# Performance work log

Measured on AMD Instinct MI355X. Metric: run time of the kernel, lower is better.

Reference implementation:

```python
import jax, jax.numpy as jnp
import numpy as np

B, N, C, Cn, M = 4, 4096, 32, 64, 64


def fps(event, npoint):
    """Farthest point sampling, faithful to farthest_point_sample_batch.
    Returns selected points in ORIGINAL index order (masked_select semantics).
    event: [B, n, c] -> [B, npoint, c]
    """
    b, n, c = event.shape
    bidx = jnp.arange(b)
    barycenter = jnp.mean(event, axis=1, keepdims=True)            # [B,1,c]
    d0 = jnp.sum((event - barycenter) ** 2, axis=-1)               # [B,n]
    farthest = jnp.argmax(d0, axis=1)                              # [B]
    distance = jnp.full((b, n), 1e10, dtype=event.dtype)
    sel = jnp.zeros((b, n), dtype=bool)

    def body(carry, _):
        distance, farthest, sel = carry
        sel = sel.at[bidx, farthest].set(True)
        centroid = jnp.take_along_axis(event, farthest[:, None, None], axis=1)  # [B,1,c]
        d = jnp.sum((event - centroid) ** 2, axis=-1)              # [B,n]
        distance = jnp.minimum(distance, d)
        farthest = jnp.argmax(distance, axis=1)
        return (distance, farthest, sel), None

    (distance, farthest, sel), _ = jax.lax.scan(
        body, (distance, farthest, sel), None, length=npoint)
    # masked_select keeps original index order: stable sort puts selected first
    order = jnp.argsort(~sel, axis=1, stable=True)[:, :npoint]     # [B,npoint]
    return jnp.take_along_axis(event, order[:, :, None], axis=1)   # [B,npoint,c]


def setup_inputs() -> dict:
    key = jax.random.key(0)
    ks = jax.random.split(key, 7)
    s = 0.1
    return {
        "events_feature": jax.random.normal(ks[0], (B, N, C), jnp.float32),
        "W_qs": jax.random.normal(ks[1], (Cn, C), jnp.float32) * s,
        "W_ks": jax.random.normal(ks[2], (Cn, C), jnp.float32) * s,
        "W_vs": jax.random.normal(ks[3], (Cn, C), jnp.float32) * s,
        "W_pe": jax.random.normal(ks[4], (Cn, C), jnp.float32) * s,
        "W_sa1": jax.random.normal(ks[5], (1, Cn), jnp.float32) * s,
        "W_sa2": jax.random.normal(ks[6], (C, Cn), jnp.float32) * s,
    }


def reference(events_feature, W_qs, W_ks, W_vs, W_pe, W_sa1, W_sa2):
    q = events_feature @ W_qs.T                                   # [B,N,Cn]
    k = events_feature @ W_ks.T                                   # [B,N,Cn]
    v = events_feature @ W_vs.T                                   # [B,N,Cn]

    # position encoding: pairwise diff to M FPS-sampled events, then C->Cn
    ev_m = fps(events_feature, M)                                 # [B,M,C]
    pe = events_feature[:, :, None, :] - ev_m[:, None, :, :]      # [B,N,M,C]
    pe = pe @ W_pe.T                                              # [B,N,M,Cn]

    k_m = fps(k, M)                                               # [B,M,Cn]
    v_m = fps(v, M)                                               # [B,M,Cn]

    # vector attention scores: (q - k_m + pe) -> scalar per (n,m)
    sa = q[:, :, None, :] - k_m[:, None, :, :] + pe               # [B,N,M,Cn]
    logits = jnp.squeeze(sa @ W_sa1.T, -1)                        # [B,N,M]
    scores = jax.nn.softmax(logits, axis=-1)                      # [B,N,M]

    # Original: matmul(scores[B,1,N,M], (v_multi+pe).permute->[B,Cn,M,N]) then
    # sum over last axis. Summing first over n' is the same math and avoids the
    # [B,Cn,N,N] intermediate: sum_{n'} v_multi = N * v_m; sum_{n'} pe.
    S = N * v_m + jnp.sum(pe, axis=1)                             # [B,M,Cn]
    attn = jnp.einsum('bnm,bmc->bnc', scores, S)                  # [B,N,Cn]
    return attn @ W_sa2.T                                         # [B,N,C]
```

## Files before the change

### kernel.cpp

```cpp
#include <hip/hip_runtime.h>

constexpr int N_ = 4096, C_ = 32, CN_ = 64, M_ = 64;
constexpr int TPB = 1024;
constexpr int RPT = 3, LPT = 1;
constexpr int NREG = RPT * TPB;
constexpr int NLDS = N_ - NREG;
constexpr int NWAVES = TPB / 64;
constexpr int NTPB = 256;
constexpr int NCHUNK = N_ / NTPB;

typedef float v2f  __attribute__((ext_vector_type(2)));
typedef float v16f __attribute__((ext_vector_type(16)));

#define PKFMA(acc, zz, cc) \
  asm("v_pk_fma_f32 %0, %1, %2, %0" : "+v"(acc) : "v"(zz), "s"(cc))

__device__ __forceinline__ unsigned fmap(float v) {
  unsigned u = __float_as_uint(v);
  u ^= (unsigned)((int)u >> 31) | 0x80000000u;
  return u;
}

__device__ __forceinline__ float rfl(float v) {
  return __uint_as_float(__builtin_amdgcn_readfirstlane(__float_as_uint(v)));
}

template <int CTRL, int RM>
__device__ __forceinline__ unsigned long long kmax_dpp(unsigned long long k) {
  int lo = (int)(unsigned)k, hi = (int)(unsigned)(k >> 32);
  int plo = __builtin_amdgcn_update_dpp(lo, lo, CTRL, RM, 0xf, false);
  int phi = __builtin_amdgcn_update_dpp(hi, hi, CTRL, RM, 0xf, false);
  unsigned long long p =
      ((unsigned long long)(unsigned)phi << 32) | (unsigned)plo;
  return p > k ? p : k;
}

__device__ __forceinline__ unsigned long long wave_kmax(unsigned long long k) {
  k = kmax_dpp<0x111, 0xF>(k);
  k = kmax_dpp<0x112, 0xF>(k);
  k = kmax_dpp<0x114, 0xF>(k);
  k = kmax_dpp<0x118, 0xF>(k);
  k = kmax_dpp<0x142, 0xA>(k);
  k = kmax_dpp<0x143, 0xC>(k);
  return k;
}

__global__ __attribute__((amdgpu_flat_work_group_size(NTPB, NTPB),
                          amdgpu_waves_per_eu(1, 4)))
void norms_kernel(
    const float* __restrict__ ev, const float* __restrict__ Wk,
    const float* __restrict__ Wv, float* __restrict__ nrm_all,
    float* __restrict__ zall, float* __restrict__ partials) {
  int blk = blockIdx.x;
  int chunk = blk & (NCHUNK - 1), br = blk >> 4;
  int r = br % 3, b = br / 3;
  int t = threadIdx.x;
  __shared__ float G[C_][C_ + 1];
  const float* W = (r == 1) ? Wk : Wv;
  for (int e = t; e < C_ * C_; e += NTPB) {
    int a = e >> 5, d = e & 31;
    float g;
    if (r == 0) {
      g = (a == d) ? 1.f : 0.f;
    } else {
      double acc = 0.0;
      for (int q = 0; q < CN_; ++q)
        acc += (double)W[q * C_ + a] * (double)W[q * C_ + d];
      g = (float)acc;
    }
    G[a][d] = g;
  }
  __syncthreads();
  int p = chunk * NTPB + t;
  const float4* row = (const float4*)(ev + ((size_t)b * N_ + p) * C_);
  float x[C_];
#pragma unroll
  for (int q = 0; q < C_ / 4; ++q) {
    float4 v = row[q];
    x[q * 4 + 0] = v.x; x[q * 4 + 1] = v.y; x[q * 4 + 2] = v.z; x[q * 4 + 3] = v.w;
  }
  double n = 0.0;
  float z[C_];
#pragma unroll
  for (int a = 0; a < C_; ++a) {
    double ta = 0.0;
#pragma unroll
    for (int d = 0; d < C_; ++d) ta += (double)G[a][d] * (double)x[d];
    z[a] = (float)ta;
    n += ta * (double)x[a];
  }
  nrm_all[(size_t)br * N_ + p] = (float)n;
  float4* zrow = (float4*)(zall + ((size_t)br * N_ + p) * C_);
#pragma unroll
  for (int q = 0; q < C_ / 4; ++q)
    zrow[q] = make_float4(z[q * 4 + 0], z[q * 4 + 1], z[q * 4 + 2], z[q * 4 + 3]);

  if (r == 0) {
    __shared__ float msum[NTPB / 64][C_];
#pragma unroll
    for (int d = 0; d < C_; ++d) {
      float s = x[d];
#pragma unroll
      for (int off = 32; off; off >>= 1) s += __shfl_xor(s, off);
      if ((t & 63) == 0) msum[t >> 6][d] = s;
    }
    __syncthreads();
    if (t < C_)
      partials[((size_t)b * NCHUNK + chunk) * C_ + t] =
          msum[0][t] + msum[1][t] + msum[2][t] + msum[3][t];
  }
}

__global__ __attribute__((amdgpu_flat_work_group_size(TPB, TPB),
                          amdgpu_waves_per_eu(4, 4)))
void fps_kernel(
    const float* __restrict__ ev, const float* __restrict__ nrm_all,
    const float* __restrict__ zall, const float* __restrict__ partials,
    int* __restrict__ idx_ws) {
  const int t = threadIdx.x;
  const int blk = blockIdx.x;
  const int b = blk / 3;
  const float* evb = ev + (size_t)b * N_ * C_;
  const float* nrm = nrm_all + (size_t)blk * N_;
  const float4* zb4 = (const float4*)(zall + (size_t)blk * N_ * C_);

  __shared__ float LP[C_ / 4][NLDS][4];
  __shared__ float cf0[C_];
  __shared__ unsigned long long redK[2][NWAVES];

  v2f z2[RPT][C_ / 2];
  float pn[RPT], dmin[RPT];
  float nl, dminL;

#pragma unroll
  for (int j = 0; j < RPT; ++j) {
    int p = j * TPB + t;
#pragma unroll
    for (int q = 0; q < C_ / 4; ++q) {
      float4 v = zb4[(size_t)p * 8 + q];
      z2[j][2 * q + 0] = v2f{v.x, v.y};
      z2[j][2 * q + 1] = v2f{v.z, v.w};
    }
    pn[j] = nrm[p];
    dmin[j] = 1e10f;
  }
  {
    int p = NREG + t;
#pragma unroll
    for (int q = 0; q < C_ / 4; ++q) {
      float4 v = zb4[(size_t)p * 8 + q];
      *(float4*)&LP[q][t][0] = v;
    }
    nl = nrm[p];
    dminL = 1e10f;
  }
  if (t < C_) {
    float s = 0.f;
#pragma unroll
    for (int c = 0; c < NCHUNK; ++c) s += partials[((size_t)b * NCHUNK + c) * C_ + t];
    cf0[t] = s * (1.f / (float)N_);
  }
  __syncthreads();

  auto eval = [&](const v2f (&csp)[C_ / 2], float curN,
                  bool update) -> unsigned long long {
    v2f a0 = {0.f, 0.f}, a1 = {0.f, 0.f}, a2 = {0.f, 0.f}, aL = {0.f, 0.f};
#pragma unroll
    for (int q = 0; q < C_ / 4; ++q) {
      float4 l = *(const float4*)&LP[q][t][0];
      v2f l0 = {l.x, l.y}, l1 = {l.z, l.w};
      PKFMA(a0, z2[0][2 * q + 0], csp[2 * q + 0]);
      PKFMA(a0, z2[0][2 * q + 1], csp[2 * q + 1]);
      PKFMA(a1, z2[1][2 * q + 0], csp[2 * q + 0]);
      PKFMA(a1, z2[1][2 * q + 1], csp[2 * q + 1]);
      PKFMA(a2, z2[2][2 * q + 0], csp[2 * q + 0]);
      PKFMA(a2, z2[2][2 * q + 1], csp[2 * q + 1]);
      PKFMA(aL, l0, csp[2 * q + 0]);
      PKFMA(aL, l1, csp[2 * q + 1]);
    }
    float acc[RPT] = {a0.x + a0.y, a1.x + a1.y, a2.x + a2.y};
    float bv = -3e38f; int bi = 0;
#pragma unroll
    for (int j = 0; j < RPT; ++j) {
      float d = fmaf(-2.f, acc[j], pn[j]) + curN;
      float v;
      if (update) { dmin[j] = fminf(dmin[j], d); v = dmin[j]; }
      else v = d;
      if (v > bv) { bv = v; bi = j * TPB + t; }
    }
    {
      float d = fmaf(-2.f, aL.x + aL.y, nl) + curN;
      float v;
      if (update) { dminL = fminf(dminL, d); v = dminL; }
      else v = d;
      if (v > bv) { bv = v; bi = NREG + t; }
    }
    unsigned long long k =
        ((unsigned long long)fmap(bv) << 12) | (unsigned)(4095 - bi);
    return wave_kmax(k);
  };

  {
    v2f csp[C_ / 2];
#pragma unroll
    for (int i = 0; i < C_ / 2; ++i)
      csp[i] = v2f{rfl(cf0[2 * i]), rfl(cf0[2 * i + 1])};
    unsigned long long k = eval(csp, 0.f, false);
    if ((t & 63) == 63) redK[0][t >> 6] = k;
  }
  __syncthreads();

  for (int it = 0; it < M_; ++it) {
    int rb = it & 1;
    unsigned long long k = redK[rb][t & (NWAVES - 1)];
    k = kmax_dpp<0x111, 0xF>(k);
    k = kmax_dpp<0x112, 0xF>(k);
    k = kmax_dpp<0x114, 0xF>(k);
    k = kmax_dpp<0x118, 0xF>(k);
    unsigned klo = (unsigned)__builtin_amdgcn_readlane((int)(unsigned)k, 15);
    int jsel = 4095 - (int)(klo & 4095u);
    if (t == 0) idx_ws[blk * M_ + it] = jsel;
    if (jsel < NREG) {
      if ((jsel & (TPB - 1)) == t) {
        int j = jsel >> 10;
        if (j == 0) dmin[0] = -3e38f;
        else if (j == 1) dmin[1] = -3e38f;
        else dmin[2] = -3e38f;
      }
    } else {
      if (jsel - NREG == t) dminL = -3e38f;
    }
    if (it == M_ - 1) break;
    const float* cfp = evb + (size_t)jsel * C_;
    const float* nrmp = nrm + jsel;
    v16f cs0, cs1; float curN;
    asm volatile(
        "s_load_dwordx16 %0, %3, 0\n\t"
        "s_load_dwordx16 %1, %3, 64\n\t"
        "s_load_dword %2, %4, 0\n\t"
        "s_waitcnt lgkmcnt(0)"
        : "=&s"(cs0), "=&s"(cs1), "=&s"(curN)
        : "s"(cfp), "s"(nrmp));
    v2f csp[C_ / 2];
#pragma unroll
    for (int i = 0; i < 8; ++i) {
      csp[i]     = v2f{cs0[2 * i], cs0[2 * i + 1]};
      csp[8 + i] = v2f{cs1[2 * i], cs1[2 * i + 1]};
    }
    unsigned long long kk = eval(csp, curN, true);
    if ((t & 63) == 63) redK[rb ^ 1][t >> 6] = kk;
    __syncthreads();
  }
}

__global__ __launch_bounds__(256, 1) void finalize_kernel(
    const float* __restrict__ ev, const float* __restrict__ Wk,
    const float* __restrict__ Wv, const float* __restrict__ Wpe,
    const float* __restrict__ Wsa1, const float* __restrict__ Wsa2,
    const int* __restrict__ idx_ws, const float* __restrict__ partials,
    float* __restrict__ outvec_ws) {
  const int b = blockIdx.x;
  const int t = threadIdx.x;
  const float* evb = ev + (size_t)b * N_ * C_;

  __shared__ float Wl[3][CN_][C_];
  __shared__ float W1l[CN_];
  __shared__ float W2l[C_][CN_ + 1];
  __shared__ int   lidx[3][M_], sidx[3][M_];
  __shared__ float XP[3][M_][C_];
  __shared__ float PRJ[3][M_][CN_ + 1];
  __shared__ float sumx[C_], Pl[CN_], sl[M_], TP[4][CN_];

  {
    const float* Ws[3] = {Wpe, Wk, Wv};
#pragma unroll
    for (int r = 0; r < 3; ++r)
      for (int i = t; i < CN_ * C_ / 4; i += 256)
        ((float4*)&Wl[r][0][0])[i] = ((const float4*)Ws[r])[i];
    if (t < CN_) W1l[t] = Wsa1[t];
    for (int i = t; i < C_ * CN_; i += 256)
      W2l[i >> 6][i & 63] = Wsa2[i];
  }
  if (t < 192) {
    int r = t >> 6, mm = t & 63;
    lidx[r][mm] = idx_ws[(b * 3 + r) * M_ + mm];
  }
  if (t < C_) {
    float s = 0.f;
#pragma unroll
    for (int c = 0; c < NCHUNK; ++c) s += partials[((size_t)b * NCHUNK + c) * C_ + t];
    sumx[t] = s;
  }
  __syncthreads();
  if (t < 192) {
    int r = t >> 6, mm = t & 63;
    int my = lidx[r][mm];
    int rank = 0;
#pragma unroll
    for (int j = 0; j < M_; ++j)
      rank += (lidx[r][j] < my) || (lidx[r][j] == my && j < mm);
    sidx[r][rank] = my;
  }
  __syncthreads();
  for (int g = t; g < 3 * M_ * 8; g += 256) {
    int row = g >> 3, q = g & 7;
    int r = row >> 6, m = row & 63;
    int pi = sidx[r][m];
    *(float4*)&XP[r][m][q * 4] = ((const float4*)(evb + (size_t)pi * C_))[q];
  }
  __syncthreads();
  {
    int w = t >> 6, cn = t & 63;
    if (w < 3) {
      float wr[C_];
#pragma unroll
      for (int q = 0; q < C_ / 4; ++q) {
        float4 v = *(const float4*)&Wl[w][cn][q * 4];
        wr[q * 4 + 0] = v.x; wr[q * 4 + 1] = v.y;
        wr[q * 4 + 2] = v.z; wr[q * 4 + 3] = v.w;
      }
      for (int m = 0; m < M_; ++m) {
        float a = 0.f;
#pragma unroll
        for (int q = 0; q < C_ / 4; ++q) {
          float4 x = *(const float4*)&XP[w][m][q * 4];
          a = fmaf(x.x, wr[q * 4 + 0], a);
          a = fmaf(x.y, wr[q * 4 + 1], a);
          a = fmaf(x.z, wr[q * 4 + 2], a);
          a = fmaf(x.w, wr[q * 4 + 3], a);
        }
        PRJ[w][m][cn] = a;
      }
    } else {
      float a = 0.f;
#pragma unroll
      for (int c = 0; c < C_; ++c) a = fmaf(sumx[c], Wl[0][cn][c], a);
      Pl[cn] = a;
    }
  }
  __syncthreads();
  if (t < 64) {
    float cm = 0.f;
#pragma unroll 8
    for (int cn = 0; cn < CN_; ++cn)
      cm = fmaf(PRJ[1][t][cn] + PRJ[0][t][cn], W1l[cn], cm);
    float lg = -cm;
    float mx = lg;
#pragma unroll
    for (int off = 32; off; off >>= 1) mx = fmaxf(mx, __shfl_xor(mx, off));
    float e = expf(lg - mx);
    float ssum = e;
#pragma unroll
    for (int off = 32; off; off >>= 1) ssum += __shfl_xor(ssum, off);
    sl[t] = e / ssum;
  }
  __syncthreads();
  {
    int cn = t & 63, h = t >> 6;
    float a = 0.f;
#pragma unroll
    for (int i = 0; i < 16; ++i) {
      int mm = h * 16 + i;
      a = fmaf(sl[mm],
               fmaf((float)N_, PRJ[2][mm][cn], Pl[cn]) - (float)N_ * PRJ[0][mm][cn],
               a);
    }
    TP[h][cn] = a;
  }
  __syncthreads();
  if (t < C_) {
    float o = 0.f;
#pragma unroll 8
    for (int cn = 0; cn < CN_; ++cn) {
      float tv = TP[0][cn] + TP[1][cn] + TP[2][cn] + TP[3][cn];
      o = fmaf(tv, W2l[t][cn], o);
    }
    outvec_ws[b * C_ + t] = o;
  }
}

__global__ void bcast_kernel(const float* __restrict__ outvec_ws,
                             float4* __restrict__ out) {
  int i = blockIdx.x * 256 + threadIdx.x;
  int b = i >> 15;
  int j = i & 7;
  const float4* ov = (const float4*)outvec_ws;
  out[i] = ov[b * 8 + j];
}

extern "C" void kernel_launch(void* const* d_in, const int* in_sizes, int n_in,
                              void* d_out, int out_size, void* d_ws, size_t ws_size,
                              hipStream_t stream) {
  const float* ev   = (const float*)d_in[0];
  const float* Wk   = (const float*)d_in[2];
  const float* Wv   = (const float*)d_in[3];
  const float* Wpe  = (const float*)d_in[4];
  const float* Wsa1 = (const float*)d_in[5];
  const float* Wsa2 = (const float*)d_in[6];
  float* out = (float*)d_out;

  char* ws = (char*)d_ws;
  int*   idx    = (int*)ws;
  float* parts  = (float*)(ws + 3072);
  float* outvec = (float*)(ws + 11264);
  float* nrm    = (float*)(ws + 11776);
  float* zall   = (float*)(ws + 208384);

  norms_kernel   <<<dim3(192), dim3(NTPB), 0, stream>>>(ev, Wk, Wv, nrm, zall, parts);
  fps_kernel     <<<dim3(12),  dim3(TPB),  0, stream>>>(ev, nrm, zall, parts, idx);
  finalize_kernel<<<dim3(4),   dim3(256),  0, stream>>>(ev, Wk, Wv, Wpe, Wsa1, Wsa2,
                                                        idx, parts, outvec);
  bcast_kernel   <<<dim3(512), dim3(256),  0, stream>>>(outvec, (float4*)out);
}
```

Before: 156.7 us.

## Shrink FPS block to 256 threads with 13 register and 3 LDS points each

```diff
diff --git a/kernel.cpp b/kernel.cpp
--- a/kernel.cpp
+++ b/kernel.cpp
@@ -1,8 +1,8 @@
 #include <hip/hip_runtime.h>
 
 constexpr int N_ = 4096, C_ = 32, CN_ = 64, M_ = 64;
-constexpr int TPB = 1024;
-constexpr int RPT = 3, LPT = 1;
+constexpr int TPB = 256;
+constexpr int RPT = 13, LPT = 3;
 constexpr int NREG = RPT * TPB;
 constexpr int NLDS = N_ - NREG;
 constexpr int NWAVES = TPB / 64;
@@ -112,7 +112,7 @@
 }
 
 __global__ __attribute__((amdgpu_flat_work_group_size(TPB, TPB),
-                          amdgpu_waves_per_eu(4, 4)))
+                          amdgpu_waves_per_eu(1, 1)))
 void fps_kernel(
     const float* __restrict__ ev, const float* __restrict__ nrm_all,
     const float* __restrict__ zall, const float* __restrict__ partials,
@@ -130,7 +130,7 @@
 
   v2f z2[RPT][C_ / 2];
   float pn[RPT], dmin[RPT];
-  float nl, dminL;
+  float nl[LPT], dminL[LPT];
 
 #pragma unroll
   for (int j = 0; j < RPT; ++j) {
@@ -144,15 +144,17 @@
     pn[j] = nrm[p];
     dmin[j] = 1e10f;
   }
-  {
-    int p = NREG + t;
+#pragma unroll
+  for (int i = 0; i < LPT; ++i) {
+    int col = i * TPB + t;
+    int p = NREG + col;
 #pragma unroll
     for (int q = 0; q < C_ / 4; ++q) {
       float4 v = zb4[(size_t)p * 8 + q];
-      *(float4*)&LP[q][t][0] = v;
-    }
-    nl = nrm[p];
-    dminL = 1e10f;
+      *(float4*)&LP[q][col][0] = v;
+    }
+    nl[i] = nrm[p];
+    dminL[i] = 1e10f;
   }
   if (t < C_) {
     float s = 0.f;
@@ -164,36 +166,42 @@
 
   auto eval = [&](const v2f (&csp)[C_ / 2], float curN,
                   bool update) -> unsigned long long {
-    v2f a0 = {0.f, 0.f}, a1 = {0.f, 0.f}, a2 = {0.f, 0.f}, aL = {0.f, 0.f};
+    v2f a[RPT], aL[LPT];
+#pragma unroll
+    for (int j = 0; j < RPT; ++j) a[j] = v2f{0.f, 0.f};
+#pragma unroll
+    for (int i = 0; i < LPT; ++i) aL[i] = v2f{0.f, 0.f};
 #pragma unroll
     for (int q = 0; q < C_ / 4; ++q) {
-      float4 l = *(const float4*)&LP[q][t][0];
-      v2f l0 = {l.x, l.y}, l1 = {l.z, l.w};
-      PKFMA(a0, z2[0][2 * q + 0], csp[2 * q + 0]);
-      PKFMA(a0, z2[0][2 * q + 1], csp[2 * q + 1]);
-      PKFMA(a1, z2[1][2 * q + 0], csp[2 * q + 0]);
-      PKFMA(a1, z2[1][2 * q + 1], csp[2 * q + 1]);
-      PKFMA(a2, z2[2][2 * q + 0], csp[2 * q + 0]);
-      PKFMA(a2, z2[2][2 * q + 1], csp[2 * q + 1]);
-      PKFMA(aL, l0, csp[2 * q + 0]);
-      PKFMA(aL, l1, csp[2 * q + 1]);
-    }
-    float acc[RPT] = {a0.x + a0.y, a1.x + a1.y, a2.x + a2.y};
+#pragma unroll
+      for (int i = 0; i < LPT; ++i) {
+        float4 l = *(const float4*)&LP[q][i * TPB + t][0];
+        v2f l0 = {l.x, l.y}, l1 = {l.z, l.w};
+        PKFMA(aL[i], l0, csp[2 * q + 0]);
+        PKFMA(aL[i], l1, csp[2 * q + 1]);
+      }
+#pragma unroll
+      for (int j = 0; j < RPT; ++j) {
+        PKFMA(a[j], z2[j][2 * q + 0], csp[2 * q + 0]);
+        PKFMA(a[j], z2[j][2 * q + 1], csp[2 * q + 1]);
+      }
+    }
     float bv = -3e38f; int bi = 0;
 #pragma unroll
     for (int j = 0; j < RPT; ++j) {
-      float d = fmaf(-2.f, acc[j], pn[j]) + curN;
+      float d = fmaf(-2.f, a[j].x + a[j].y, pn[j]) + curN;
       float v;
       if (update) { dmin[j] = fminf(dmin[j], d); v = dmin[j]; }
       else v = d;
       if (v > bv) { bv = v; bi = j * TPB + t; }
     }
-    {
-      float d = fmaf(-2.f, aL.x + aL.y, nl) + curN;
+#pragma unroll
+    for (int i = 0; i < LPT; ++i) {
+      float d = fmaf(-2.f, aL[i].x + aL[i].y, nl[i]) + curN;
       float v;
-      if (update) { dminL = fminf(dminL, d); v = dminL; }
+      if (update) { dminL[i] = fminf(dminL[i], d); v = dminL[i]; }
       else v = d;
-      if (v > bv) { bv = v; bi = NREG + t; }
+      if (v > bv) { bv = v; bi = NREG + i * TPB + t; }
     }
     unsigned long long k =
         ((unsigned long long)fmap(bv) << 12) | (unsigned)(4095 - bi);
@@ -215,20 +223,24 @@
     unsigned long long k = redK[rb][t & (NWAVES - 1)];
     k = kmax_dpp<0x111, 0xF>(k);
     k = kmax_dpp<0x112, 0xF>(k);
-    k = kmax_dpp<0x114, 0xF>(k);
-    k = kmax_dpp<0x118, 0xF>(k);
-    unsigned klo = (unsigned)__builtin_amdgcn_readlane((int)(unsigned)k, 15);
+    unsigned klo = (unsigned)__builtin_amdgcn_readlane((int)(unsigned)k, 3);
     int jsel = 4095 - (int)(klo & 4095u);
     if (t == 0) idx_ws[blk * M_ + it] = jsel;
     if (jsel < NREG) {
       if ((jsel & (TPB - 1)) == t) {
-        int j = jsel >> 10;
-        if (j == 0) dmin[0] = -3e38f;
-        else if (j == 1) dmin[1] = -3e38f;
-        else dmin[2] = -3e38f;
+        int j = jsel >> 8;
+#pragma unroll
+        for (int jj = 0; jj < RPT; ++jj)
+          if (jj == j) dmin[jj] = -3e38f;
       }
     } else {
-      if (jsel - NREG == t) dminL = -3e38f;
+      int col = jsel - NREG;
+      if ((col & (TPB - 1)) == t) {
+        int i = col >> 8;
+#pragma unroll
+        for (int ii = 0; ii < LPT; ++ii)
+          if (ii == i) dminL[ii] = -3e38f;
+      }
     }
     if (it == M_ - 1) break;
     const float* cfp = evb + (size_t)jsel * C_;
```

New measurement: 221.7 us. 1.41x slower.

## Split each FPS run across eight workgroups with global atomic argmax sync

Applied to the files above, without the earlier changes.

```diff
diff --git a/kernel.cpp b/kernel.cpp
--- a/kernel.cpp
+++ b/kernel.cpp
@@ -1,11 +1,9 @@
 #include <hip/hip_runtime.h>
 
 constexpr int N_ = 4096, C_ = 32, CN_ = 64, M_ = 64;
-constexpr int TPB = 1024;
-constexpr int RPT = 3, LPT = 1;
-constexpr int NREG = RPT * TPB;
-constexpr int NLDS = N_ - NREG;
-constexpr int NWAVES = TPB / 64;
+constexpr int NWG = 8;
+constexpr int SLICE = N_ / NWG;
+constexpr int TPB = 256;
 constexpr int NTPB = 256;
 constexpr int NCHUNK = N_ / NTPB;
 
@@ -90,10 +88,13 @@
     n += ta * (double)x[a];
   }
   nrm_all[(size_t)br * N_ + p] = (float)n;
-  float4* zrow = (float4*)(zall + ((size_t)br * N_ + p) * C_);
-#pragma unroll
-  for (int q = 0; q < C_ / 4; ++q)
-    zrow[q] = make_float4(z[q * 4 + 0], z[q * 4 + 1], z[q * 4 + 2], z[q * 4 + 3]);
+  if (r != 0) {
+    float4* zrow =
+        (float4*)(zall + ((size_t)(2 * b + r - 1) * N_ + p) * C_);
+#pragma unroll
+    for (int q = 0; q < C_ / 4; ++q)
+      zrow[q] = make_float4(z[q * 4 + 0], z[q * 4 + 1], z[q * 4 + 2], z[q * 4 + 3]);
+  }
 
   if (r == 0) {
     __shared__ float msum[NTPB / 64][C_];
@@ -112,29 +113,35 @@
 }
 
 __global__ __attribute__((amdgpu_flat_work_group_size(TPB, TPB),
-                          amdgpu_waves_per_eu(4, 4)))
+                          amdgpu_waves_per_eu(1, 2)))
 void fps_kernel(
     const float* __restrict__ ev, const float* __restrict__ nrm_all,
     const float* __restrict__ zall, const float* __restrict__ partials,
-    int* __restrict__ idx_ws) {
+    int* __restrict__ idx_ws, unsigned long long* __restrict__ slotK,
+    unsigned* __restrict__ slotC) {
   const int t = threadIdx.x;
-  const int blk = blockIdx.x;
-  const int b = blk / 3;
+  const int run = blockIdx.x >> 3;
+  const int g = blockIdx.x & 7;
+  const int b = run / 3, r = run % 3;
   const float* evb = ev + (size_t)b * N_ * C_;
-  const float* nrm = nrm_all + (size_t)blk * N_;
-  const float4* zb4 = (const float4*)(zall + (size_t)blk * N_ * C_);
-
-  __shared__ float LP[C_ / 4][NLDS][4];
+  const float* nrm = nrm_all + (size_t)run * N_;
+  const float4* zb4 = (r == 0)
+      ? (const float4*)evb
+      : (const float4*)(zall + (size_t)(2 * b + r - 1) * N_ * C_);
+  unsigned long long* sK = slotK + (size_t)run * M_;
+  unsigned* sC = slotC + (size_t)run * M_;
+
   __shared__ float cf0[C_];
-  __shared__ unsigned long long redK[2][NWAVES];
-
-  v2f z2[RPT][C_ / 2];
-  float pn[RPT], dmin[RPT];
-  float nl, dminL;
-
-#pragma unroll
-  for (int j = 0; j < RPT; ++j) {
-    int p = j * TPB + t;
+  __shared__ unsigned long long redL[TPB / 64];
+  __shared__ unsigned long long bcK64;
+
+  v2f z2[2][C_ / 2];
+  float pn[2], dmin[2];
+  const int p0 = g * SLICE + t;
+
+#pragma unroll
+  for (int j = 0; j < 2; ++j) {
+    int p = p0 + j * TPB;
 #pragma unroll
     for (int q = 0; q < C_ / 4; ++q) {
       float4 v = zb4[(size_t)p * 8 + q];
@@ -144,16 +151,6 @@
     pn[j] = nrm[p];
     dmin[j] = 1e10f;
   }
-  {
-    int p = NREG + t;
-#pragma unroll
-    for (int q = 0; q < C_ / 4; ++q) {
-      float4 v = zb4[(size_t)p * 8 + q];
-      *(float4*)&LP[q][t][0] = v;
-    }
-    nl = nrm[p];
-    dminL = 1e10f;
-  }
   if (t < C_) {
     float s = 0.f;
 #pragma unroll
@@ -164,73 +161,80 @@
 
   auto eval = [&](const v2f (&csp)[C_ / 2], float curN,
                   bool update) -> unsigned long long {
-    v2f a0 = {0.f, 0.f}, a1 = {0.f, 0.f}, a2 = {0.f, 0.f}, aL = {0.f, 0.f};
-#pragma unroll
-    for (int q = 0; q < C_ / 4; ++q) {
-      float4 l = *(const float4*)&LP[q][t][0];
-      v2f l0 = {l.x, l.y}, l1 = {l.z, l.w};
-      PKFMA(a0, z2[0][2 * q + 0], csp[2 * q + 0]);
-      PKFMA(a0, z2[0][2 * q + 1], csp[2 * q + 1]);
-      PKFMA(a1, z2[1][2 * q + 0], csp[2 * q + 0]);
-      PKFMA(a1, z2[1][2 * q + 1], csp[2 * q + 1]);
-      PKFMA(a2, z2[2][2 * q + 0], csp[2 * q + 0]);
-      PKFMA(a2, z2[2][2 * q + 1], csp[2 * q + 1]);
-      PKFMA(aL, l0, csp[2 * q + 0]);
-      PKFMA(aL, l1, csp[2 * q + 1]);
-    }
-    float acc[RPT] = {a0.x + a0.y, a1.x + a1.y, a2.x + a2.y};
+    v2f a0 = {0.f, 0.f}, a1 = {0.f, 0.f};
+#pragma unroll
+    for (int i = 0; i < C_ / 2; ++i) {
+      PKFMA(a0, z2[0][i], csp[i]);
+      PKFMA(a1, z2[1][i], csp[i]);
+    }
     float bv = -3e38f; int bi = 0;
-#pragma unroll
-    for (int j = 0; j < RPT; ++j) {
-      float d = fmaf(-2.f, acc[j], pn[j]) + curN;
+    {
+      float d = fmaf(-2.f, a0.x + a0.y, pn[0]) + curN;
       float v;
-      if (update) { dmin[j] = fminf(dmin[j], d); v = dmin[j]; }
+      if (update) { dmin[0] = fminf(dmin[0], d); v = dmin[0]; }
       else v = d;
-      if (v > bv) { bv = v; bi = j * TPB + t; }
+      if (v > bv) { bv = v; bi = p0; }
     }
     {
-      float d = fmaf(-2.f, aL.x + aL.y, nl) + curN;
+      float d = fmaf(-2.f, a1.x + a1.y, pn[1]) + curN;
       float v;
-      if (update) { dminL = fminf(dminL, d); v = dminL; }
+      if (update) { dmin[1] = fminf(dmin[1], d); v = dmin[1]; }
       else v = d;
-      if (v > bv) { bv = v; bi = NREG + t; }
+      if (v > bv) { bv = v; bi = p0 + TPB; }
     }
     unsigned long long k =
         ((unsigned long long)fmap(bv) << 12) | (unsigned)(4095 - bi);
     return wave_kmax(k);
   };
 
+  auto post = [&](int s) {
+    if (t < 64) {
+      unsigned long long k = redL[t & 3];
+      k = kmax_dpp<0x111, 0xF>(k);
+      k = kmax_dpp<0x112, 0xF>(k);
+      unsigned lo = (unsigned)__builtin_amdgcn_readlane((int)(unsigned)k, 3);
+      unsigned hi = (unsigned)__builtin_amdgcn_readlane((int)(unsigned)(k >> 32), 3);
+      if (t == 0) {
+        unsigned long long kwg = ((unsigned long long)hi << 32) | lo;
+        __hip_atomic_fetch_max(&sK[s], kwg, __ATOMIC_RELAXED,
+                               __HIP_MEMORY_SCOPE_AGENT);
+        __hip_atomic_fetch_add(&sC[s], 1u, __ATOMIC_RELEASE,
+                               __HIP_MEMORY_SCOPE_AGENT);
+      }
+    }
+  };
+
   {
     v2f csp[C_ / 2];
 #pragma unroll
     for (int i = 0; i < C_ / 2; ++i)
       csp[i] = v2f{rfl(cf0[2 * i]), rfl(cf0[2 * i + 1])};
     unsigned long long k = eval(csp, 0.f, false);
-    if ((t & 63) == 63) redK[0][t >> 6] = k;
-  }
-  __syncthreads();
-
-  for (int it = 0; it < M_; ++it) {
-    int rb = it & 1;
-    unsigned long long k = redK[rb][t & (NWAVES - 1)];
-    k = kmax_dpp<0x111, 0xF>(k);
-    k = kmax_dpp<0x112, 0xF>(k);
-    k = kmax_dpp<0x114, 0xF>(k);
-    k = kmax_dpp<0x118, 0xF>(k);
-    unsigned klo = (unsigned)__builtin_amdgcn_readlane((int)(unsigned)k, 15);
-    int jsel = 4095 - (int)(klo & 4095u);
-    if (t == 0) idx_ws[blk * M_ + it] = jsel;
-    if (jsel < NREG) {
-      if ((jsel & (TPB - 1)) == t) {
-        int j = jsel >> 10;
-        if (j == 0) dmin[0] = -3e38f;
-        else if (j == 1) dmin[1] = -3e38f;
-        else dmin[2] = -3e38f;
+    if ((t & 63) == 63) redL[t >> 6] = k;
+  }
+  __syncthreads();
+  post(0);
+
+  for (int s = 0; s < M_; ++s) {
+    if (t == 0) {
+      while (__hip_atomic_load(&sC[s], __ATOMIC_ACQUIRE,
+                               __HIP_MEMORY_SCOPE_AGENT) < (unsigned)NWG)
+        __builtin_amdgcn_s_sleep(2);
+      bcK64 = __hip_atomic_load(&sK[s], __ATOMIC_RELAXED,
+                                __HIP_MEMORY_SCOPE_AGENT);
+    }
+    __syncthreads();
+    unsigned long long kf = bcK64;
+    int jsel = 4095 - (int)(kf & 4095ull);
+    if (g == 0 && t == 0) idx_ws[run * M_ + s] = jsel;
+    if ((jsel >> 9) == g) {
+      int loc = jsel & (SLICE - 1);
+      if ((loc & (TPB - 1)) == t) {
+        if (loc < TPB) dmin[0] = -3e38f;
+        else dmin[1] = -3e38f;
       }
-    } else {
-      if (jsel - NREG == t) dminL = -3e38f;
-    }
-    if (it == M_ - 1) break;
+    }
+    if (s == M_ - 1) break;
     const float* cfp = evb + (size_t)jsel * C_;
     const float* nrmp = nrm + jsel;
     v16f cs0, cs1; float curN;
@@ -248,8 +252,9 @@
       csp[8 + i] = v2f{cs1[2 * i], cs1[2 * i + 1]};
     }
     unsigned long long kk = eval(csp, curN, true);
-    if ((t & 63) == 63) redK[rb ^ 1][t >> 6] = kk;
+    if ((t & 63) == 63) redL[t >> 6] = kk;
     __syncthreads();
+    post(s + 1);
   }
 }
 
@@ -403,11 +408,16 @@
   int*   idx    = (int*)ws;
   float* parts  = (float*)(ws + 3072);
   float* outvec = (float*)(ws + 11264);
-  float* nrm    = (float*)(ws + 11776);
-  float* zall   = (float*)(ws + 208384);
-
+  unsigned long long* slotK =
+      (unsigned long long*)(ws + 11776);
+  unsigned* slotC = (unsigned*)(ws + 17920);
+  float* nrm    = (float*)(ws + 20992);
+  float* zall   = (float*)(ws + 217600);
+
+  hipMemsetAsync(ws + 11776, 0, 9216, stream);
   norms_kernel   <<<dim3(192), dim3(NTPB), 0, stream>>>(ev, Wk, Wv, nrm, zall, parts);
-  fps_kernel     <<<dim3(12),  dim3(TPB),  0, stream>>>(ev, nrm, zall, parts, idx);
+  fps_kernel     <<<dim3(96),  dim3(TPB),  0, stream>>>(ev, nrm, zall, parts, idx,
+                                                        slotK, slotC);
   finalize_kernel<<<dim3(4),   dim3(256),  0, stream>>>(ev, Wk, Wv, Wpe, Wsa1, Wsa2,
                                                         idx, parts, outvec);
   bcast_kernel   <<<dim3(512), dim3(256),  0, stream>>>(outvec, (float4*)out);
```

Result: slower. 214.5 us (+36.9%).

## Halve FPS block to 512 threads with seven register rows per thread

Applied to the files above, without the earlier changes.

```diff
diff --git a/kernel.cpp b/kernel.cpp
--- a/kernel.cpp
+++ b/kernel.cpp
@@ -1,8 +1,8 @@
 #include <hip/hip_runtime.h>
 
 constexpr int N_ = 4096, C_ = 32, CN_ = 64, M_ = 64;
-constexpr int TPB = 1024;
-constexpr int RPT = 3, LPT = 1;
+constexpr int TPB = 512;
+constexpr int RPT = 7, LPT = 1;
 constexpr int NREG = RPT * TPB;
 constexpr int NLDS = N_ - NREG;
 constexpr int NWAVES = TPB / 64;
@@ -90,10 +90,13 @@
     n += ta * (double)x[a];
   }
   nrm_all[(size_t)br * N_ + p] = (float)n;
-  float4* zrow = (float4*)(zall + ((size_t)br * N_ + p) * C_);
-#pragma unroll
-  for (int q = 0; q < C_ / 4; ++q)
-    zrow[q] = make_float4(z[q * 4 + 0], z[q * 4 + 1], z[q * 4 + 2], z[q * 4 + 3]);
+  if (r != 0) {
+    float4* zrow =
+        (float4*)(zall + ((size_t)(2 * b + r - 1) * N_ + p) * C_);
+#pragma unroll
+    for (int q = 0; q < C_ / 4; ++q)
+      zrow[q] = make_float4(z[q * 4 + 0], z[q * 4 + 1], z[q * 4 + 2], z[q * 4 + 3]);
+  }
 
   if (r == 0) {
     __shared__ float msum[NTPB / 64][C_];
@@ -112,17 +115,19 @@
 }
 
 __global__ __attribute__((amdgpu_flat_work_group_size(TPB, TPB),
-                          amdgpu_waves_per_eu(4, 4)))
+                          amdgpu_waves_per_eu(2, 2)))
 void fps_kernel(
     const float* __restrict__ ev, const float* __restrict__ nrm_all,
     const float* __restrict__ zall, const float* __restrict__ partials,
     int* __restrict__ idx_ws) {
   const int t = threadIdx.x;
-  const int blk = blockIdx.x;
-  const int b = blk / 3;
+  const int run = blockIdx.x;
+  const int b = run / 3, r = run % 3;
   const float* evb = ev + (size_t)b * N_ * C_;
-  const float* nrm = nrm_all + (size_t)blk * N_;
-  const float4* zb4 = (const float4*)(zall + (size_t)blk * N_ * C_);
+  const float* nrm = nrm_all + (size_t)run * N_;
+  const float4* zb4 = (r == 0)
+      ? (const float4*)evb
+      : (const float4*)(zall + (size_t)(2 * b + r - 1) * N_ * C_);
 
   __shared__ float LP[C_ / 4][NLDS][4];
   __shared__ float cf0[C_];
@@ -164,36 +169,44 @@
 
   auto eval = [&](const v2f (&csp)[C_ / 2], float curN,
                   bool update) -> unsigned long long {
-    v2f a0 = {0.f, 0.f}, a1 = {0.f, 0.f}, a2 = {0.f, 0.f}, aL = {0.f, 0.f};
-#pragma unroll
-    for (int q = 0; q < C_ / 4; ++q) {
-      float4 l = *(const float4*)&LP[q][t][0];
-      v2f l0 = {l.x, l.y}, l1 = {l.z, l.w};
-      PKFMA(a0, z2[0][2 * q + 0], csp[2 * q + 0]);
-      PKFMA(a0, z2[0][2 * q + 1], csp[2 * q + 1]);
-      PKFMA(a1, z2[1][2 * q + 0], csp[2 * q + 0]);
-      PKFMA(a1, z2[1][2 * q + 1], csp[2 * q + 1]);
-      PKFMA(a2, z2[2][2 * q + 0], csp[2 * q + 0]);
-      PKFMA(a2, z2[2][2 * q + 1], csp[2 * q + 1]);
-      PKFMA(aL, l0, csp[2 * q + 0]);
-      PKFMA(aL, l1, csp[2 * q + 1]);
-    }
-    float acc[RPT] = {a0.x + a0.y, a1.x + a1.y, a2.x + a2.y};
     float bv = -3e38f; int bi = 0;
-#pragma unroll
-    for (int j = 0; j < RPT; ++j) {
-      float d = fmaf(-2.f, acc[j], pn[j]) + curN;
+    auto touch_reg = [&](int j, const v2f& a) {
+      float d = fmaf(-2.f, a.x + a.y, pn[j]) + curN;
       float v;
       if (update) { dmin[j] = fminf(dmin[j], d); v = dmin[j]; }
       else v = d;
       if (v > bv) { bv = v; bi = j * TPB + t; }
-    }
+    };
     {
+      v2f aL = {0.f, 0.f}, a6 = {0.f, 0.f};
+#pragma unroll
+      for (int q = 0; q < C_ / 4; ++q) {
+        float4 l = *(const float4*)&LP[q][t][0];
+        v2f l0 = {l.x, l.y}, l1 = {l.z, l.w};
+        PKFMA(aL, l0, csp[2 * q + 0]);
+        PKFMA(aL, l1, csp[2 * q + 1]);
+        PKFMA(a6, z2[6][2 * q + 0], csp[2 * q + 0]);
+        PKFMA(a6, z2[6][2 * q + 1], csp[2 * q + 1]);
+      }
+      touch_reg(6, a6);
       float d = fmaf(-2.f, aL.x + aL.y, nl) + curN;
       float v;
       if (update) { dminL = fminf(dminL, d); v = dminL; }
       else v = d;
       if (v > bv) { bv = v; bi = NREG + t; }
+    }
+#pragma unroll
+    for (int jp = 0; jp < 6; jp += 2) {
+      v2f a0 = {0.f, 0.f}, a1 = {0.f, 0.f};
+#pragma unroll
+      for (int q = 0; q < C_ / 4; ++q) {
+        PKFMA(a0, z2[jp][2 * q + 0], csp[2 * q + 0]);
+        PKFMA(a0, z2[jp][2 * q + 1], csp[2 * q + 1]);
+        PKFMA(a1, z2[jp + 1][2 * q + 0], csp[2 * q + 0]);
+        PKFMA(a1, z2[jp + 1][2 * q + 1], csp[2 * q + 1]);
+      }
+      touch_reg(jp, a0);
+      touch_reg(jp + 1, a1);
     }
     unsigned long long k =
         ((unsigned long long)fmap(bv) << 12) | (unsigned)(4095 - bi);
@@ -216,16 +229,15 @@
     k = kmax_dpp<0x111, 0xF>(k);
     k = kmax_dpp<0x112, 0xF>(k);
     k = kmax_dpp<0x114, 0xF>(k);
-    k = kmax_dpp<0x118, 0xF>(k);
-    unsigned klo = (unsigned)__builtin_amdgcn_readlane((int)(unsigned)k, 15);
+    unsigned klo = (unsigned)__builtin_amdgcn_readlane((int)(unsigned)k, 7);
     int jsel = 4095 - (int)(klo & 4095u);
-    if (t == 0) idx_ws[blk * M_ + it] = jsel;
+    if (t == 0) idx_ws[run * M_ + it] = jsel;
     if (jsel < NREG) {
       if ((jsel & (TPB - 1)) == t) {
-        int j = jsel >> 10;
-        if (j == 0) dmin[0] = -3e38f;
-        else if (j == 1) dmin[1] = -3e38f;
-        else dmin[2] = -3e38f;
+        int j = jsel >> 9;
+#pragma unroll
+        for (int jj = 0; jj < RPT; ++jj)
+          if (jj == j) dmin[jj] = -3e38f;
       }
     } else {
       if (jsel - NREG == t) dminL = -3e38f;
```

Result: slower. 163.5 us (+4.4%).
